# Kernel tuning notes

Measured on AMD Instinct MI355X. Metric: run time of the kernel, lower is better.

The kernel has to match this reference:

```python
import jax, jax.numpy as jnp
import numpy as np

HIDDEN = 2048
INTER = 8192
RANK = 16
SPARSITY_RATIO = 0.5
MAINTAIN_CHANNELS = 10


def setup_inputs() -> dict:
    key = jax.random.key(0)
    ks = jax.random.split(key, 7)
    B, S = 4, 2048
    x1 = jax.random.normal(ks[0], (B, S, HIDDEN), dtype=jnp.float32)
    # Linear weights stored transposed (in_features, out_features), bias=False
    w_up = jax.random.normal(ks[1], (HIDDEN, INTER), dtype=jnp.float32) / np.sqrt(HIDDEN)
    w_up_lora_a = jax.random.normal(ks[2], (HIDDEN, RANK), dtype=jnp.float32) / np.sqrt(HIDDEN)
    w_up_lora_b = jax.random.normal(ks[3], (RANK, INTER), dtype=jnp.float32) / np.sqrt(RANK)
    w_down = jax.random.normal(ks[4], (INTER, HIDDEN), dtype=jnp.float32) / np.sqrt(INTER)
    w_down_lora_a = jax.random.normal(ks[5], (INTER, RANK), dtype=jnp.float32) / np.sqrt(INTER)
    w_down_lora_b = jax.random.normal(ks[6], (RANK, HIDDEN), dtype=jnp.float32) / np.sqrt(RANK)
    return {
        "x1": x1,
        "w_up": w_up,
        "w_up_lora_a": w_up_lora_a,
        "w_up_lora_b": w_up_lora_b,
        "w_down": w_down,
        "w_down_lora_a": w_down_lora_a,
        "w_down_lora_b": w_down_lora_b,
    }


def reference(x1, w_up, w_up_lora_a, w_up_lora_b, w_down, w_down_lora_a, w_down_lora_b):
    # up projection: dense + low-rank LoRA
    y1 = x1 @ w_up + (x1 @ w_up_lora_a) @ w_up_lora_b          # [B, S, I]
    x2 = jax.nn.relu(y1)                                        # activation_forward='relu'
    # down projection: dense + low-rank LoRA
    y2 = x2 @ w_down + (x2 @ w_down_lora_a) @ w_down_lora_b    # [B, S, H]
    # sparse-save path: per-channel zero counts, keep k channels with FEWEST zeros
    zero_counts = jnp.sum(x2 == 0, axis=-2)                     # [B, I]
    k = min(int(SPARSITY_RATIO * x2.shape[-1]), MAINTAIN_CHANNELS)
    _, topk_indices = jax.lax.top_k(-zero_counts, k)            # smallest counts -> [B, k]
    # per-batch gather of selected channels (replaces Python loop in original)
    x2_save = jnp.take_along_axis(x2, topk_indices[:, None, :], axis=-1)  # [B, S, k]
    return y2, x2_save
```

## Files before the change

### kernel.cpp

```cpp
#include <hip/hip_runtime.h>
#include <stdint.h>

#define HIDDEN 2048
#define INTER 8192
#define RANK 16
#define BATCH 4
#define SEQ 2048
#define MROWS (BATCH * SEQ)
#define KSAVE 10
#define FIXCAP (1u << 18)
#define FIX_TAU 1.2e-4f
#define NHALF 4096

typedef unsigned short u16;
typedef __attribute__((ext_vector_type(8))) __bf16 bf16x8;
typedef __attribute__((ext_vector_type(4))) float f32x4;

__device__ __forceinline__ float bf16_to_f32(u16 h) {
    return __uint_as_float(((unsigned int)h) << 16);
}
__device__ __forceinline__ u16 f32_to_bf16(float f) {
    unsigned int u = __float_as_uint(f);
    u += 0x7fffu + ((u >> 16) & 1u);
    return (u16)(u >> 16);
}
__device__ __forceinline__ void split_bf16(float v, u16& h, u16& l) {
    h = f32_to_bf16(v);
    l = f32_to_bf16(v - bf16_to_f32(h));
}

#define TILE_SH (128 * 32)

__device__ __forceinline__ int swz_chunk(int r, int c) {
    return r * 4 + (c ^ ((r >> 1) & 3));
}

template <int NCH>
__device__ __forceinline__ void stage_tileN(const u16* g, int ldk, u16* lds, int tid) {
    int wid = tid >> 6, lane = tid & 63;
#pragma unroll
    for (int c0 = 0; c0 < NCH; c0 += 512) {
        int ch = c0 + wid * 64 + lane;
        int r = ch >> 2;
        int c = (ch & 3) ^ ((r >> 1) & 3);
        const u16* src = g + (size_t)r * ldk + c * 8;
        u16* dst = lds + (size_t)(c0 + wid * 64) * 8;
        __builtin_amdgcn_global_load_lds(
            (const __attribute__((address_space(1))) void*)src,
            (__attribute__((address_space(3))) void*)dst, 16, 0, 0);
    }
}

__device__ __forceinline__ bf16x8 read_frag(const u16* lds, int r, int q) {
    return *(const bf16x8*)(lds + swz_chunk(r, q) * 8);
}

__global__ __launch_bounds__(512) void gemm_up_mfma3(
    const float* __restrict__ x1,
    const u16* __restrict__ wth, const u16* __restrict__ wtl,
    const float* __restrict__ t1, const float* __restrict__ upB,
    u16* __restrict__ x2, int* __restrict__ counts,
    unsigned* __restrict__ fixctr, unsigned* __restrict__ fixlist,
    int noff)
{
    __shared__ u16 Ah[TILE_SH], Al[TILE_SH];
    __shared__ u16 Bh[2 * TILE_SH], Bl[2 * TILE_SH];
    int tid = threadIdx.x, lane = tid & 63, wid = tid >> 6;
    int wr = wid >> 2, wc = wid & 3;
    int col = lane & 15, q = lane >> 4;

    int bid = blockIdx.y * gridDim.x + blockIdx.x;
    int g = bid >> 8, within = bid & 255;
    int nb = g * 4 + (within & 3);
    int mb = within >> 2;
    int m0 = mb * 128, n0l = nb * 256, n0g = noff + n0l;

    f32x4 acc[4][4];
#pragma unroll
    for (int i = 0; i < 4; ++i)
#pragma unroll
        for (int j = 0; j < 4; ++j) acc[i][j] = (f32x4){0.f, 0.f, 0.f, 0.f};

    const float* ga = x1 + (size_t)m0 * HIDDEN;
    const u16* gb_h = wth + (size_t)n0l * HIDDEN;
    const u16* gb_l = wtl + (size_t)n0l * HIDDEN;
    int f4 = tid & 7;
    int rA = tid >> 3;

    for (int k0 = 0; k0 < HIDDEN; k0 += 32) {
        stage_tileN<1024>(gb_h + k0, HIDDEN, Bh, tid);
        stage_tileN<1024>(gb_l + k0, HIDDEN, Bl, tid);
#pragma unroll
        for (int h = 0; h < 2; ++h) {
            int row = rA + h * 64;
            float4 v = *(const float4*)(ga + (size_t)row * HIDDEN + k0 + f4 * 4);
            unsigned hx0 = __float_as_uint(v.x) & 0xffff0000u;
            unsigned hx1 = __float_as_uint(v.y) & 0xffff0000u;
            unsigned hx2 = __float_as_uint(v.z) & 0xffff0000u;
            unsigned hx3 = __float_as_uint(v.w) & 0xffff0000u;
            float l0 = v.x - __uint_as_float(hx0);
            float l1 = v.y - __uint_as_float(hx1);
            float l2 = v.z - __uint_as_float(hx2);
            float l3 = v.w - __uint_as_float(hx3);
            unsigned lo0 = __float_as_uint(l0) & 0xffff0000u;
            unsigned lo1 = __float_as_uint(l1) & 0xffff0000u;
            unsigned lo2 = __float_as_uint(l2) & 0xffff0000u;
            unsigned lo3 = __float_as_uint(l3) & 0xffff0000u;
            uint2 hp = {(hx0 >> 16) | hx1, (hx2 >> 16) | hx3};
            uint2 lp = {(lo0 >> 16) | lo1, (lo2 >> 16) | lo3};
            int pos = swz_chunk(row, f4 >> 1) * 8 + (f4 & 1) * 4;
            *(uint2*)(Ah + pos) = hp;
            *(uint2*)(Al + pos) = lp;
        }
        __syncthreads();
        bf16x8 ah[4], al[4];
#pragma unroll
        for (int i = 0; i < 4; ++i) {
            int r = wr * 64 + i * 16 + col;
            ah[i] = read_frag(Ah, r, q);
            al[i] = read_frag(Al, r, q);
        }
#pragma unroll
        for (int j = 0; j < 4; ++j) {
            int rr = wc * 64 + j * 16 + col;
            bf16x8 bh = read_frag(Bh, rr, q);
            bf16x8 bl = read_frag(Bl, rr, q);
#pragma unroll
            for (int i = 0; i < 4; ++i) {
                acc[i][j] = __builtin_amdgcn_mfma_f32_16x16x32_bf16(ah[i], bh, acc[i][j], 0, 0, 0);
                acc[i][j] = __builtin_amdgcn_mfma_f32_16x16x32_bf16(al[i], bh, acc[i][j], 0, 0, 0);
                acc[i][j] = __builtin_amdgcn_mfma_f32_16x16x32_bf16(ah[i], bl, acc[i][j], 0, 0, 0);
            }
        }
        __syncthreads();
    }

    for (int idx = tid; idx < 4096; idx += 512) {
        int r = idx >> 5, c16 = idx & 31;
        float tv = (c16 < RANK) ? t1[(size_t)(m0 + r) * RANK + c16] : 0.f;
        u16 th, tl2;
        split_bf16(tv, th, tl2);
        int pos = swz_chunk(r, c16 >> 3) * 8 + (c16 & 7);
        Ah[pos] = th; Al[pos] = tl2;
    }
    for (int idx = tid; idx < 8192; idx += 512) {
        int r = idx >> 5, c16 = idx & 31;
        float uv = (c16 < RANK) ? upB[(size_t)c16 * INTER + n0g + r] : 0.f;
        u16 uh, ul;
        split_bf16(uv, uh, ul);
        int pos = swz_chunk(r, c16 >> 3) * 8 + (c16 & 7);
        Bh[pos] = uh; Bl[pos] = ul;
    }
    __syncthreads();
    {
        bf16x8 ah[4], al[4];
#pragma unroll
        for (int i = 0; i < 4; ++i) {
            int r = wr * 64 + i * 16 + col;
            ah[i] = read_frag(Ah, r, q);
            al[i] = read_frag(Al, r, q);
        }
#pragma unroll
        for (int j = 0; j < 4; ++j) {
            int rr = wc * 64 + j * 16 + col;
            bf16x8 bh = read_frag(Bh, rr, q);
            bf16x8 bl = read_frag(Bl, rr, q);
#pragma unroll
            for (int i = 0; i < 4; ++i) {
                acc[i][j] = __builtin_amdgcn_mfma_f32_16x16x32_bf16(ah[i], bh, acc[i][j], 0, 0, 0);
                acc[i][j] = __builtin_amdgcn_mfma_f32_16x16x32_bf16(al[i], bh, acc[i][j], 0, 0, 0);
                acc[i][j] = __builtin_amdgcn_mfma_f32_16x16x32_bf16(ah[i], bl, acc[i][j], 0, 0, 0);
            }
        }
    }

    int b = m0 >> 11;
#pragma unroll
    for (int j = 0; j < 4; ++j) {
        int n = n0g + wc * 64 + j * 16 + col;
        int zc = 0;
#pragma unroll
        for (int i = 0; i < 4; ++i) {
#pragma unroll
            for (int reg = 0; reg < 4; ++reg) {
                int m = m0 + wr * 64 + i * 16 + q * 4 + reg;
                float v = acc[i][j][reg];
                if (fabsf(v) < FIX_TAU) {
                    unsigned slot = atomicAdd(fixctr, 1u);
                    if (slot < FIXCAP) fixlist[slot] = ((unsigned)m << 13) | (unsigned)n;
                }
                zc += (v <= 0.f) ? 1 : 0;
                float rv = v > 0.f ? v : 0.f;
                x2[(size_t)m * INTER + n] = f32_to_bf16(rv);
            }
        }
        zc += __shfl_down(zc, 32);
        zc += __shfl_down(zc, 16);
        if (lane < 16) atomicAdd(&counts[b * INTER + n], zc);
    }
}

__global__ __launch_bounds__(512) void gemm_down_mfma2(
    const u16* __restrict__ x2, const u16* __restrict__ wdt,
    const float* __restrict__ t2, const float* __restrict__ dnB,
    float* __restrict__ out)
{
    __shared__ u16 As[TILE_SH];
    __shared__ u16 Bs[2 * TILE_SH];
    int tid = threadIdx.x, lane = tid & 63, wid = tid >> 6;
    int wr = wid >> 2, wc = wid & 3;
    int col = lane & 15, q = lane >> 4;
    int m0 = blockIdx.y * 128, n0 = blockIdx.x * 256;

    f32x4 acc[4][4];
#pragma unroll
    for (int i = 0; i < 4; ++i)
#pragma unroll
        for (int j = 0; j < 4; ++j) acc[i][j] = (f32x4){0.f, 0.f, 0.f, 0.f};

    const u16* ga = x2 + (size_t)m0 * INTER;
    const u16* gb = wdt + (size_t)n0 * INTER;

    for (int k0 = 0; k0 < INTER; k0 += 32) {
        stage_tileN<512>(ga + k0, INTER, As, tid);
        stage_tileN<1024>(gb + k0, INTER, Bs, tid);
        __syncthreads();
        bf16x8 af[4];
#pragma unroll
        for (int i = 0; i < 4; ++i) af[i] = read_frag(As, wr * 64 + i * 16 + col, q);
#pragma unroll
        for (int j = 0; j < 4; ++j) {
            bf16x8 bf = read_frag(Bs, wc * 64 + j * 16 + col, q);
#pragma unroll
            for (int i = 0; i < 4; ++i)
                acc[i][j] = __builtin_amdgcn_mfma_f32_16x16x32_bf16(af[i], bf, acc[i][j], 0, 0, 0);
        }
        __syncthreads();
    }

    for (int idx = tid; idx < 4096; idx += 512) {
        int r = idx >> 5, c16 = idx & 31;
        float tv = (c16 < RANK) ? t2[(size_t)(m0 + r) * RANK + c16] : 0.f;
        int pos = swz_chunk(r, c16 >> 3) * 8 + (c16 & 7);
        As[pos] = f32_to_bf16(tv);
    }
    for (int idx = tid; idx < 8192; idx += 512) {
        int r = idx >> 5, c16 = idx & 31;
        float uv = (c16 < RANK) ? dnB[(size_t)c16 * HIDDEN + n0 + r] : 0.f;
        int pos = swz_chunk(r, c16 >> 3) * 8 + (c16 & 7);
        Bs[pos] = f32_to_bf16(uv);
    }
    __syncthreads();
    {
        bf16x8 af[4];
#pragma unroll
        for (int i = 0; i < 4; ++i) af[i] = read_frag(As, wr * 64 + i * 16 + col, q);
#pragma unroll
        for (int j = 0; j < 4; ++j) {
            bf16x8 bf = read_frag(Bs, wc * 64 + j * 16 + col, q);
#pragma unroll
            for (int i = 0; i < 4; ++i)
                acc[i][j] = __builtin_amdgcn_mfma_f32_16x16x32_bf16(af[i], bf, acc[i][j], 0, 0, 0);
        }
    }
#pragma unroll
    for (int i = 0; i < 4; ++i)
#pragma unroll
        for (int j = 0; j < 4; ++j) {
            int n = n0 + wc * 64 + j * 16 + col;
#pragma unroll
            for (int reg = 0; reg < 4; ++reg) {
                int m = m0 + wr * 64 + i * 16 + q * 4 + reg;
                out[(size_t)m * HIDDEN + n] = acc[i][j][reg];
            }
        }
}

__global__ __launch_bounds__(256) void fixup_kernel(
    const float* __restrict__ x1, const float* __restrict__ w_up,
    const float* __restrict__ t1, const float* __restrict__ upB,
    const unsigned* __restrict__ fixctr, const unsigned* __restrict__ fixlist,
    u16* __restrict__ x2, int* __restrict__ counts)
{
    unsigned n_items = *fixctr;
    if (n_items > FIXCAP) n_items = FIXCAP;
    int lane = threadIdx.x & 63;
    int gwave = blockIdx.x * 4 + (threadIdx.x >> 6);
    int nwaves = gridDim.x * 4;
    for (unsigned it = gwave; it < n_items; it += nwaves) {
        unsigned code = fixlist[it];
        int m = code >> 13, n = code & 8191;
        float s = 0.f;
        const float* xr = x1 + (size_t)m * HIDDEN;
        for (int k = lane; k < HIDDEN; k += 64)
            s = fmaf(xr[k], w_up[(size_t)k * INTER + n], s);
#pragma unroll
        for (int off = 32; off > 0; off >>= 1) s += __shfl_down(s, off);
        if (lane == 0) {
            float lo = 0.f;
#pragma unroll
            for (int r = 0; r < RANK; ++r)
                lo = fmaf(t1[(size_t)m * RANK + r], upB[(size_t)r * INTER + n], lo);
            float y = s + lo;
            int oldz = (x2[(size_t)m * INTER + n] == 0) ? 1 : 0;
            int newz = (y <= 0.f) ? 1 : 0;
            if (newz != oldz) atomicAdd(&counts[(m >> 11) * INTER + n], newz - oldz);
            x2[(size_t)m * INTER + n] = f32_to_bf16(y > 0.f ? y : 0.f);
        }
    }
}

template <bool SPLIT>
__global__ __launch_bounds__(256) void transpose_cvt(
    const float* __restrict__ in, u16* __restrict__ outh, u16* __restrict__ outl,
    int R, int C)
{
    __shared__ float t[32][33];
    int x = threadIdx.x & 31, y = threadIdx.x >> 5;
    int r0 = blockIdx.y * 32, c0 = blockIdx.x * 32;
#pragma unroll
    for (int p = 0; p < 4; ++p)
        t[y + p * 8][x] = in[(size_t)(r0 + y + p * 8) * C + c0 + x];
    __syncthreads();
#pragma unroll
    for (int p = 0; p < 4; ++p) {
        float v = t[x][y + p * 8];
        u16 h = f32_to_bf16(v);
        outh[(size_t)(c0 + y + p * 8) * R + r0 + x] = h;
        if (SPLIT)
            outl[(size_t)(c0 + y + p * 8) * R + r0 + x] = f32_to_bf16(v - bf16_to_f32(h));
    }
}

__global__ __launch_bounds__(256) void rowdot16_f32(
    const float* __restrict__ X, const float* __restrict__ A,
    float* __restrict__ T, int K)
{
    __shared__ float red[256][RANK + 1];
    int m = blockIdx.x;
    const float* xr = X + (size_t)m * K;
    float acc[RANK];
#pragma unroll
    for (int r = 0; r < RANK; ++r) acc[r] = 0.f;
    for (int k = threadIdx.x; k < K; k += 256) {
        float xv = xr[k];
        const float* ar = A + (size_t)k * RANK;
#pragma unroll
        for (int r = 0; r < RANK; ++r) acc[r] = fmaf(xv, ar[r], acc[r]);
    }
#pragma unroll
    for (int r = 0; r < RANK; ++r) red[threadIdx.x][r] = acc[r];
    __syncthreads();
    for (int off = 128; off > 0; off >>= 1) {
        if (threadIdx.x < off) {
#pragma unroll
            for (int r = 0; r < RANK; ++r)
                red[threadIdx.x][r] += red[threadIdx.x + off][r];
        }
        __syncthreads();
    }
    if (threadIdx.x < RANK) T[(size_t)m * RANK + threadIdx.x] = red[0][threadIdx.x];
}

__global__ __launch_bounds__(256) void rowdot16_bf16(
    const u16* __restrict__ X, const float* __restrict__ A,
    float* __restrict__ T, int K)
{
    __shared__ float red[256][RANK + 1];
    int m = blockIdx.x;
    const u16* xr = X + (size_t)m * K;
    float acc[RANK];
#pragma unroll
    for (int r = 0; r < RANK; ++r) acc[r] = 0.f;
    for (int k = threadIdx.x * 8; k < K; k += 256 * 8) {
        uint4 p = *(const uint4*)(xr + k);
        unsigned w_[4] = {p.x, p.y, p.z, p.w};
#pragma unroll
        for (int e = 0; e < 4; ++e) {
            float v0 = bf16_to_f32((u16)(w_[e] & 0xffffu));
            float v1 = bf16_to_f32((u16)(w_[e] >> 16));
            const float* ar0 = A + (size_t)(k + 2 * e) * RANK;
            const float* ar1 = A + (size_t)(k + 2 * e + 1) * RANK;
#pragma unroll
            for (int r = 0; r < RANK; ++r)
                acc[r] = fmaf(v0, ar0[r], fmaf(v1, ar1[r], acc[r]));
        }
    }
#pragma unroll
    for (int r = 0; r < RANK; ++r) red[threadIdx.x][r] = acc[r];
    __syncthreads();
    for (int off = 128; off > 0; off >>= 1) {
        if (threadIdx.x < off) {
#pragma unroll
            for (int r = 0; r < RANK; ++r)
                red[threadIdx.x][r] += red[threadIdx.x + off][r];
        }
        __syncthreads();
    }
    if (threadIdx.x < RANK) T[(size_t)m * RANK + threadIdx.x] = red[0][threadIdx.x];
}

#define BM 128
#define BN 128
#define BK 16
#define TM 8

__global__ __launch_bounds__(256) void gemm_up_f32(
    const float* __restrict__ A, const float* __restrict__ B,
    const float* __restrict__ Tl, const float* __restrict__ Bl,
    u16* __restrict__ C, int M, int N, int K)
{
    __shared__ float As[BK][BM + 4];
    __shared__ float Bs[BK][BN];
    int tid = threadIdx.x;
    int tx = tid % 16, ty = tid / 16;
    int m0 = blockIdx.y * BM, n0 = blockIdx.x * BN;
    const float* Ab = A + (size_t)m0 * K;
    const float* Bb = B + n0;
    float acc[TM][8];
#pragma unroll
    for (int i = 0; i < TM; ++i)
#pragma unroll
        for (int j = 0; j < 8; ++j) acc[i][j] = 0.f;

    int arow = tid >> 2, acol = (tid & 3) * 4;
    int brow = tid >> 5, bcol = (tid & 31) * 4;

    for (int k0 = 0; k0 < K; k0 += BK) {
#pragma unroll
        for (int h = 0; h < 2; ++h) {
            int r = arow + h * 64;
            float4 v = *(const float4*)(Ab + (size_t)r * K + k0 + acol);
            As[acol + 0][r] = v.x; As[acol + 1][r] = v.y;
            As[acol + 2][r] = v.z; As[acol + 3][r] = v.w;
        }
#pragma unroll
        for (int h = 0; h < 2; ++h) {
            int r = brow + h * 8;
            float4 v = *(const float4*)(Bb + (size_t)(k0 + r) * N + bcol);
            *(float4*)&Bs[r][bcol] = v;
        }
        __syncthreads();
#pragma unroll
        for (int kk = 0; kk < BK; ++kk) {
            float a[TM], b[8];
#pragma unroll
            for (int i = 0; i < TM; i += 4) *(float4*)&a[i] = *(const float4*)&As[kk][ty * TM + i];
            *(float4*)&b[0] = *(const float4*)&Bs[kk][tx * 4];
            *(float4*)&b[4] = *(const float4*)&Bs[kk][64 + tx * 4];
#pragma unroll
            for (int i = 0; i < TM; ++i)
#pragma unroll
                for (int j = 0; j < 8; ++j)
                    acc[i][j] = fmaf(a[i], b[j], acc[i][j]);
        }
        __syncthreads();
    }
#pragma unroll
    for (int r = 0; r < RANK; ++r) {
        float bv[8];
#pragma unroll
        for (int j = 0; j < 4; ++j) {
            bv[j]     = Bl[(size_t)r * N + n0 + tx * 4 + j];
            bv[4 + j] = Bl[(size_t)r * N + n0 + 64 + tx * 4 + j];
        }
#pragma unroll
        for (int i = 0; i < TM; ++i) {
            float tv = Tl[(size_t)(m0 + ty * TM + i) * RANK + r];
#pragma unroll
            for (int j = 0; j < 8; ++j) acc[i][j] = fmaf(tv, bv[j], acc[i][j]);
        }
    }
#pragma unroll
    for (int i = 0; i < TM; ++i) {
        int m = m0 + ty * TM + i;
        float v[8];
#pragma unroll
        for (int j = 0; j < 8; ++j) { float x = acc[i][j]; v[j] = x > 0.f ? x : 0.f; }
        uint2 p0, p1;
        p0.x = (unsigned)f32_to_bf16(v[0]) | ((unsigned)f32_to_bf16(v[1]) << 16);
        p0.y = (unsigned)f32_to_bf16(v[2]) | ((unsigned)f32_to_bf16(v[3]) << 16);
        p1.x = (unsigned)f32_to_bf16(v[4]) | ((unsigned)f32_to_bf16(v[5]) << 16);
        p1.y = (unsigned)f32_to_bf16(v[6]) | ((unsigned)f32_to_bf16(v[7]) << 16);
        *(uint2*)(C + (size_t)m * N + n0 + tx * 4) = p0;
        *(uint2*)(C + (size_t)m * N + n0 + 64 + tx * 4) = p1;
    }
}

__global__ __launch_bounds__(256) void gemm_down_f32(
    const u16* __restrict__ A, const float* __restrict__ B,
    const float* __restrict__ Tl, const float* __restrict__ Bl,
    float* __restrict__ C, int M, int N, int K)
{
    __shared__ float As[BK][BM + 4];
    __shared__ float Bs[BK][BN];
    int tid = threadIdx.x;
    int tx = tid % 16, ty = tid / 16;
    int m0 = blockIdx.y * BM, n0 = blockIdx.x * BN;
    const u16* Ab = A + (size_t)m0 * K;
    const float* Bb = B + n0;
    float acc[TM][8];
#pragma unroll
    for (int i = 0; i < TM; ++i)
#pragma unroll
        for (int j = 0; j < 8; ++j) acc[i][j] = 0.f;

    int arow = tid >> 1, ahalf = (tid & 1) * 8;
    int brow = tid >> 5, bcol = (tid & 31) * 4;

    for (int k0 = 0; k0 < K; k0 += BK) {
        {
            uint4 v = *(const uint4*)(Ab + (size_t)arow * K + k0 + ahalf);
            unsigned int w_[4] = {v.x, v.y, v.z, v.w};
#pragma unroll
            for (int qq = 0; qq < 4; ++qq) {
                As[ahalf + 2 * qq + 0][arow] = bf16_to_f32((u16)(w_[qq] & 0xffffu));
                As[ahalf + 2 * qq + 1][arow] = bf16_to_f32((u16)(w_[qq] >> 16));
            }
        }
#pragma unroll
        for (int h = 0; h < 2; ++h) {
            int r = brow + h * 8;
            float4 v = *(const float4*)(Bb + (size_t)(k0 + r) * N + bcol);
            *(float4*)&Bs[r][bcol] = v;
        }
        __syncthreads();
#pragma unroll
        for (int kk = 0; kk < BK; ++kk) {
            float a[TM], b[8];
#pragma unroll
            for (int i = 0; i < TM; i += 4) *(float4*)&a[i] = *(const float4*)&As[kk][ty * TM + i];
            *(float4*)&b[0] = *(const float4*)&Bs[kk][tx * 4];
            *(float4*)&b[4] = *(const float4*)&Bs[kk][64 + tx * 4];
#pragma unroll
            for (int i = 0; i < TM; ++i)
#pragma unroll
                for (int j = 0; j < 8; ++j)
                    acc[i][j] = fmaf(a[i], b[j], acc[i][j]);
        }
        __syncthreads();
    }
#pragma unroll
    for (int r = 0; r < RANK; ++r) {
        float bv[8];
#pragma unroll
        for (int j = 0; j < 4; ++j) {
            bv[j]     = Bl[(size_t)r * N + n0 + tx * 4 + j];
            bv[4 + j] = Bl[(size_t)r * N + n0 + 64 + tx * 4 + j];
        }
#pragma unroll
        for (int i = 0; i < TM; ++i) {
            float tv = Tl[(size_t)(m0 + ty * TM + i) * RANK + r];
#pragma unroll
            for (int j = 0; j < 8; ++j) acc[i][j] = fmaf(tv, bv[j], acc[i][j]);
        }
    }
#pragma unroll
    for (int i = 0; i < TM; ++i) {
        int m = m0 + ty * TM + i;
        *(float4*)(C + (size_t)m * N + n0 + tx * 4)      = *(float4*)&acc[i][0];
        *(float4*)(C + (size_t)m * N + n0 + 64 + tx * 4) = *(float4*)&acc[i][4];
    }
}

__global__ __launch_bounds__(256) void gemm_down_mfma(
    const u16* __restrict__ x2, const u16* __restrict__ wdt,
    const float* __restrict__ t2, const float* __restrict__ dnB,
    float* __restrict__ out)
{
    __shared__ u16 As[TILE_SH], Bs[TILE_SH];
    int tid = threadIdx.x, lane = tid & 63, wid = tid >> 6;
    int wr = wid >> 1, wc = wid & 1;
    int col = lane & 15, q = lane >> 4;
    int m0 = blockIdx.y * 128, n0 = blockIdx.x * 128;

    f32x4 acc[4][4];
#pragma unroll
    for (int i = 0; i < 4; ++i)
#pragma unroll
        for (int j = 0; j < 4; ++j) acc[i][j] = (f32x4){0.f, 0.f, 0.f, 0.f};

    const u16* ga = x2 + (size_t)m0 * INTER;
    const u16* gb = wdt + (size_t)n0 * INTER;

    for (int k0 = 0; k0 < INTER; k0 += 32) {
        {
            int wid4 = tid >> 6, lane4 = tid & 63;
#pragma unroll
            for (int h = 0; h < 2; ++h) {
                int ch = h * 256 + wid4 * 64 + lane4;
                int r = ch >> 2;
                int c = (ch & 3) ^ ((r >> 1) & 3);
                const u16* srcA = ga + k0 + (size_t)r * INTER + c * 8;
                u16* dstA = As + (size_t)(h * 256 + wid4 * 64) * 8;
                __builtin_amdgcn_global_load_lds(
                    (const __attribute__((address_space(1))) void*)srcA,
                    (__attribute__((address_space(3))) void*)dstA, 16, 0, 0);
                const u16* srcB = gb + k0 + (size_t)r * INTER + c * 8;
                u16* dstB = Bs + (size_t)(h * 256 + wid4 * 64) * 8;
                __builtin_amdgcn_global_load_lds(
                    (const __attribute__((address_space(1))) void*)srcB,
                    (__attribute__((address_space(3))) void*)dstB, 16, 0, 0);
            }
        }
        __syncthreads();
        bf16x8 af[4];
#pragma unroll
        for (int i = 0; i < 4; ++i) af[i] = read_frag(As, wr * 64 + i * 16 + col, q);
#pragma unroll
        for (int j = 0; j < 4; ++j) {
            bf16x8 bf = read_frag(Bs, wc * 64 + j * 16 + col, q);
#pragma unroll
            for (int i = 0; i < 4; ++i)
                acc[i][j] = __builtin_amdgcn_mfma_f32_16x16x32_bf16(af[i], bf, acc[i][j], 0, 0, 0);
        }
        __syncthreads();
    }
    for (int idx = tid; idx < 128 * 32; idx += 256) {
        int r = idx >> 5, c16 = idx & 31;
        float tv = (c16 < RANK) ? t2[(size_t)(m0 + r) * RANK + c16] : 0.f;
        float uv = (c16 < RANK) ? dnB[(size_t)c16 * HIDDEN + n0 + r] : 0.f;
        int pos = swz_chunk(r, c16 >> 3) * 8 + (c16 & 7);
        As[pos] = f32_to_bf16(tv);
        Bs[pos] = f32_to_bf16(uv);
    }
    __syncthreads();
    {
        bf16x8 af[4];
#pragma unroll
        for (int i = 0; i < 4; ++i) af[i] = read_frag(As, wr * 64 + i * 16 + col, q);
#pragma unroll
        for (int j = 0; j < 4; ++j) {
            bf16x8 bf = read_frag(Bs, wc * 64 + j * 16 + col, q);
#pragma unroll
            for (int i = 0; i < 4; ++i)
                acc[i][j] = __builtin_amdgcn_mfma_f32_16x16x32_bf16(af[i], bf, acc[i][j], 0, 0, 0);
        }
    }
#pragma unroll
    for (int i = 0; i < 4; ++i)
#pragma unroll
        for (int j = 0; j < 4; ++j) {
            int n = n0 + wc * 64 + j * 16 + col;
#pragma unroll
            for (int reg = 0; reg < 4; ++reg) {
                int m = m0 + wr * 64 + i * 16 + q * 4 + reg;
                out[(size_t)m * HIDDEN + n] = acc[i][j][reg];
            }
        }
}

__global__ __launch_bounds__(256) void count_zeros(
    const u16* __restrict__ X2, int* __restrict__ counts)
{
    int i = blockIdx.x * 256 + threadIdx.x;
    int b = blockIdx.y;
    int s0 = blockIdx.z * 256;
    const u16* p = X2 + ((size_t)(b * SEQ + s0)) * INTER + i;
    int c = 0;
    for (int s = 0; s < 256; ++s) c += (p[(size_t)s * INTER] == 0) ? 1 : 0;
    atomicAdd(&counts[b * INTER + i], c);
}

__global__ __launch_bounds__(256) void topk10(
    const int* __restrict__ counts, int* __restrict__ topidx)
{
    __shared__ int keys[INTER];
    __shared__ int red[256];
    int b = blockIdx.x;
    for (int i = threadIdx.x; i < INTER; i += 256)
        keys[i] = (counts[b * INTER + i] << 13) | i;
    __syncthreads();
    for (int sel = 0; sel < KSAVE; ++sel) {
        int best = 0x7fffffff;
        for (int i = threadIdx.x; i < INTER; i += 256)
            best = min(best, keys[i]);
        red[threadIdx.x] = best;
        __syncthreads();
        for (int off = 128; off > 0; off >>= 1) {
            if (threadIdx.x < off) red[threadIdx.x] = min(red[threadIdx.x], red[threadIdx.x + off]);
            __syncthreads();
        }
        int bestkey = red[0];
        if (threadIdx.x == 0) {
            topidx[b * KSAVE + sel] = bestkey & 0x1fff;
            keys[bestkey & 0x1fff] = 0x7fffffff;
        }
        __syncthreads();
    }
}

__global__ __launch_bounds__(256) void gather_save(
    const u16* __restrict__ X2, const int* __restrict__ topidx,
    float* __restrict__ out2)
{
    int t = blockIdx.x * 256 + threadIdx.x;
    if (t >= BATCH * SEQ * KSAVE) return;
    int j = t % KSAVE;
    int s = (t / KSAVE) % SEQ;
    int b = t / (KSAVE * SEQ);
    int idx = topidx[b * KSAVE + j];
    out2[t] = bf16_to_f32(X2[((size_t)(b * SEQ + s)) * INTER + idx]);
}

extern "C" void kernel_launch(void* const* d_in, const int* in_sizes, int n_in,
                              void* d_out, int out_size, void* d_ws, size_t ws_size,
                              hipStream_t stream)
{
    const float* x1   = (const float*)d_in[0];
    const float* w_up = (const float*)d_in[1];
    const float* upA  = (const float*)d_in[2];
    const float* upB  = (const float*)d_in[3];
    const float* w_dn = (const float*)d_in[4];
    const float* dnA  = (const float*)d_in[5];
    const float* dnB  = (const float*)d_in[6];
    float* out = (float*)d_out;
    char* ws = (char*)d_ws;

    const size_t X2B   = (size_t)MROWS * INTER * 2;
    const size_t WHALF = (size_t)NHALF * HIDDEN * 2;
    const size_t WSPL  = (size_t)HIDDEN * INTER * 2;
    const size_t TB    = (size_t)MROWS * RANK * 4;
    const size_t CNTB  = (size_t)BATCH * INTER * 4;

    size_t fast_need = X2B + 2 * WHALF + 2 * TB + CNTB + 512 + 4 * (size_t)FIXCAP;
    size_t mid_need  = X2B + WSPL + 2 * TB + CNTB + 512;

    u16* x2 = (u16*)ws;
    size_t off = X2B;

    if (ws_size >= fast_need) {
        u16* wth = (u16*)(ws + off);            off += WHALF;
        u16* wtl = (u16*)(ws + off);            off += WHALF;
        float* t1 = (float*)(ws + off);         off += TB;
        float* t2 = (float*)(ws + off);         off += TB;
        int* counts = (int*)(ws + off);         off += CNTB;
        int* topidx = (int*)(ws + off);         off += 256;
        unsigned* fixctr = (unsigned*)(ws + off); off += 256;
        unsigned* fixlist = (unsigned*)(ws + off);
        u16* wdt = wth;

        hipMemsetAsync(counts, 0, CNTB, stream);
        hipMemsetAsync(fixctr, 0, 4, stream);

        rowdot16_f32<<<MROWS, 256, 0, stream>>>(x1, upA, t1, HIDDEN);

        for (int half = 0; half < 2; ++half) {
            int noff = half * NHALF;
            transpose_cvt<true><<<dim3(NHALF / 32, HIDDEN / 32), 256, 0, stream>>>(
                w_up + noff, wth, wtl, HIDDEN, INTER);
            gemm_up_mfma3<<<dim3(NHALF / 256, MROWS / 128), 512, 0, stream>>>(
                x1, wth, wtl, t1, upB, x2, counts, fixctr, fixlist, noff);
        }
        fixup_kernel<<<256, 256, 0, stream>>>(x1, w_up, t1, upB, fixctr, fixlist, x2, counts);

        topk10<<<BATCH, 256, 0, stream>>>(counts, topidx);
        gather_save<<<(BATCH * SEQ * KSAVE + 255) / 256, 256, 0, stream>>>(
            x2, topidx, out + (size_t)MROWS * HIDDEN);

        transpose_cvt<false><<<dim3(HIDDEN / 32, INTER / 32), 256, 0, stream>>>(
            w_dn, wdt, nullptr, INTER, HIDDEN);
        rowdot16_bf16<<<MROWS, 256, 0, stream>>>(x2, dnA, t2, INTER);
        gemm_down_mfma2<<<dim3(HIDDEN / 256, MROWS / 128), 512, 0, stream>>>(
            x2, wdt, t2, dnB, out);
    } else if (ws_size >= mid_need) {
        u16* wdt = (u16*)(ws + off);            off += WSPL;
        float* t1 = (float*)(ws + off);         off += TB;
        float* t2 = (float*)(ws + off);         off += TB;
        int* counts = (int*)(ws + off);         off += CNTB;
        int* topidx = (int*)(ws + off);

        hipMemsetAsync(counts, 0, CNTB, stream);
        rowdot16_f32<<<MROWS, 256, 0, stream>>>(x1, upA, t1, HIDDEN);
        gemm_up_f32<<<dim3(INTER / BN, MROWS / BM), 256, 0, stream>>>(
            x1, w_up, t1, upB, x2, MROWS, INTER, HIDDEN);
        count_zeros<<<dim3(INTER / 256, BATCH, SEQ / 256), 256, 0, stream>>>(x2, counts);
        topk10<<<BATCH, 256, 0, stream>>>(counts, topidx);
        gather_save<<<(BATCH * SEQ * KSAVE + 255) / 256, 256, 0, stream>>>(
            x2, topidx, out + (size_t)MROWS * HIDDEN);
        transpose_cvt<false><<<dim3(HIDDEN / 32, INTER / 32), 256, 0, stream>>>(
            w_dn, wdt, nullptr, INTER, HIDDEN);
        rowdot16_bf16<<<MROWS, 256, 0, stream>>>(x2, dnA, t2, INTER);
        gemm_down_mfma<<<dim3(HIDDEN / 128, MROWS / 128), 256, 0, stream>>>(
            x2, wdt, t2, dnB, out);
    } else {
        float* t1 = (float*)(ws + off);         off += TB;
        float* t2 = (float*)(ws + off);         off += TB;
        int* counts = (int*)(ws + off);         off += CNTB;
        int* topidx = (int*)(ws + off);

        hipMemsetAsync(counts, 0, CNTB, stream);
        rowdot16_f32<<<MROWS, 256, 0, stream>>>(x1, upA, t1, HIDDEN);
        gemm_up_f32<<<dim3(INTER / BN, MROWS / BM), 256, 0, stream>>>(
            x1, w_up, t1, upB, x2, MROWS, INTER, HIDDEN);
        count_zeros<<<dim3(INTER / 256, BATCH, SEQ / 256), 256, 0, stream>>>(x2, counts);
        topk10<<<BATCH, 256, 0, stream>>>(counts, topidx);
        gather_save<<<(BATCH * SEQ * KSAVE + 255) / 256, 256, 0, stream>>>(
            x2, topidx, out + (size_t)MROWS * HIDDEN);
        rowdot16_bf16<<<MROWS, 256, 0, stream>>>(x2, dnA, t2, INTER);
        gemm_down_f32<<<dim3(HIDDEN / BN, MROWS / BM), 256, 0, stream>>>(
            x2, w_dn, t2, dnB, out, MROWS, HIDDEN, INTER);
    }
}
```

Before: 2.258 ms.

## Shrink up-GEMM tile to 128x128 and replace LoRA rowdots with thread-per-row kernels

The up-projection GEMM moves from 512 threads with 128x256 tiles to 256 threads with 128x128 tiles. This halves LDS use per block and doubles the block count, and the A-tile global loads are now batched before conversion. The LoRA rank-16 projections switch from block-per-row reductions to thread-per-row kernels: split-K with a combine pass for t1, and split-K with atomics for t2. The mid-path rowdot kernel is simplified to scalar loads. The change also shrinks the fixup capacity, which risks overflow if many elements need fixing, and the atomics make t2 accumulation order nondeterministic.

```diff
diff --git a/kernel.cpp b/kernel.cpp
--- a/kernel.cpp
+++ b/kernel.cpp
@@ -8,7 +8,7 @@
 #define SEQ 2048
 #define MROWS (BATCH * SEQ)
 #define KSAVE 10
-#define FIXCAP (1u << 18)
+#define FIXCAP (1u << 16)
 #define FIX_TAU 1.2e-4f
 #define NHALF 4096
 
@@ -33,6 +33,20 @@
 
 __device__ __forceinline__ int swz_chunk(int r, int c) {
     return r * 4 + (c ^ ((r >> 1) & 3));
+}
+
+__device__ __forceinline__ void stage_tile256(const u16* g, int ldk, u16* lds, int wid, int lane) {
+#pragma unroll
+    for (int h = 0; h < 2; ++h) {
+        int ch = h * 256 + wid * 64 + lane;
+        int r = ch >> 2;
+        int c = (ch & 3) ^ ((r >> 1) & 3);
+        const u16* src = g + (size_t)r * ldk + c * 8;
+        u16* dst = lds + (size_t)(h * 256 + wid * 64) * 8;
+        __builtin_amdgcn_global_load_lds(
+            (const __attribute__((address_space(1))) void*)src,
+            (__attribute__((address_space(3))) void*)dst, 16, 0, 0);
+    }
 }
 
 template <int NCH>
@@ -55,7 +69,7 @@
     return *(const bf16x8*)(lds + swz_chunk(r, q) * 8);
 }
 
-__global__ __launch_bounds__(512) void gemm_up_mfma3(
+__global__ __launch_bounds__(256) void gemm_up_mfma2(
     const float* __restrict__ x1,
     const u16* __restrict__ wth, const u16* __restrict__ wtl,
     const float* __restrict__ t1, const float* __restrict__ upB,
@@ -63,17 +77,16 @@
     unsigned* __restrict__ fixctr, unsigned* __restrict__ fixlist,
     int noff)
 {
-    __shared__ u16 Ah[TILE_SH], Al[TILE_SH];
-    __shared__ u16 Bh[2 * TILE_SH], Bl[2 * TILE_SH];
+    __shared__ u16 Ah[TILE_SH], Al[TILE_SH], Bh[TILE_SH], Bl[TILE_SH];
     int tid = threadIdx.x, lane = tid & 63, wid = tid >> 6;
-    int wr = wid >> 2, wc = wid & 3;
+    int wr = wid >> 1, wc = wid & 1;
     int col = lane & 15, q = lane >> 4;
 
     int bid = blockIdx.y * gridDim.x + blockIdx.x;
-    int g = bid >> 8, within = bid & 255;
-    int nb = g * 4 + (within & 3);
-    int mb = within >> 2;
-    int m0 = mb * 128, n0l = nb * 256, n0g = noff + n0l;
+    int g = bid >> 9, within = bid & 511;
+    int nb = g * 8 + (within & 7);
+    int mb = within >> 3;
+    int m0 = mb * 128, n0l = nb * 128, n0g = noff + n0l;
 
     f32x4 acc[4][4];
 #pragma unroll
@@ -88,20 +101,23 @@
     int rA = tid >> 3;
 
     for (int k0 = 0; k0 < HIDDEN; k0 += 32) {
-        stage_tileN<1024>(gb_h + k0, HIDDEN, Bh, tid);
-        stage_tileN<1024>(gb_l + k0, HIDDEN, Bl, tid);
-#pragma unroll
-        for (int h = 0; h < 2; ++h) {
-            int row = rA + h * 64;
-            float4 v = *(const float4*)(ga + (size_t)row * HIDDEN + k0 + f4 * 4);
-            unsigned hx0 = __float_as_uint(v.x) & 0xffff0000u;
-            unsigned hx1 = __float_as_uint(v.y) & 0xffff0000u;
-            unsigned hx2 = __float_as_uint(v.z) & 0xffff0000u;
-            unsigned hx3 = __float_as_uint(v.w) & 0xffff0000u;
-            float l0 = v.x - __uint_as_float(hx0);
-            float l1 = v.y - __uint_as_float(hx1);
-            float l2 = v.z - __uint_as_float(hx2);
-            float l3 = v.w - __uint_as_float(hx3);
+        stage_tile256(gb_h + k0, HIDDEN, Bh, wid, lane);
+        stage_tile256(gb_l + k0, HIDDEN, Bl, wid, lane);
+        float4 v[4];
+#pragma unroll
+        for (int h = 0; h < 4; ++h)
+            v[h] = *(const float4*)(ga + (size_t)(rA + h * 32) * HIDDEN + k0 + f4 * 4);
+#pragma unroll
+        for (int h = 0; h < 4; ++h) {
+            int row = rA + h * 32;
+            unsigned hx0 = __float_as_uint(v[h].x) & 0xffff0000u;
+            unsigned hx1 = __float_as_uint(v[h].y) & 0xffff0000u;
+            unsigned hx2 = __float_as_uint(v[h].z) & 0xffff0000u;
+            unsigned hx3 = __float_as_uint(v[h].w) & 0xffff0000u;
+            float l0 = v[h].x - __uint_as_float(hx0);
+            float l1 = v[h].y - __uint_as_float(hx1);
+            float l2 = v[h].z - __uint_as_float(hx2);
+            float l3 = v[h].w - __uint_as_float(hx3);
             unsigned lo0 = __float_as_uint(l0) & 0xffff0000u;
             unsigned lo1 = __float_as_uint(l1) & 0xffff0000u;
             unsigned lo2 = __float_as_uint(l2) & 0xffff0000u;
@@ -135,21 +151,15 @@
         __syncthreads();
     }
 
-    for (int idx = tid; idx < 4096; idx += 512) {
+    for (int idx = tid; idx < 4096; idx += 256) {
         int r = idx >> 5, c16 = idx & 31;
         float tv = (c16 < RANK) ? t1[(size_t)(m0 + r) * RANK + c16] : 0.f;
-        u16 th, tl2;
+        float uv = (c16 < RANK) ? upB[(size_t)c16 * INTER + n0g + r] : 0.f;
+        u16 th, tl2, uh, ul;
         split_bf16(tv, th, tl2);
-        int pos = swz_chunk(r, c16 >> 3) * 8 + (c16 & 7);
-        Ah[pos] = th; Al[pos] = tl2;
-    }
-    for (int idx = tid; idx < 8192; idx += 512) {
-        int r = idx >> 5, c16 = idx & 31;
-        float uv = (c16 < RANK) ? upB[(size_t)c16 * INTER + n0g + r] : 0.f;
-        u16 uh, ul;
         split_bf16(uv, uh, ul);
         int pos = swz_chunk(r, c16 >> 3) * 8 + (c16 & 7);
-        Bh[pos] = uh; Bl[pos] = ul;
+        Ah[pos] = th; Al[pos] = tl2; Bh[pos] = uh; Bl[pos] = ul;
     }
     __syncthreads();
     {
@@ -310,6 +320,70 @@
     }
 }
 
+__global__ __launch_bounds__(256) void lora_t1_part(
+    const float* __restrict__ X, const float* __restrict__ A,
+    float* __restrict__ Tpart)
+{
+    int m = blockIdx.x * 256 + threadIdx.x;
+    int k0 = blockIdx.y * (HIDDEN / 2);
+    const float* xr = X + (size_t)m * HIDDEN + k0;
+    const float* Ab = A + (size_t)k0 * RANK;
+    float acc[RANK];
+#pragma unroll
+    for (int r = 0; r < RANK; ++r) acc[r] = 0.f;
+    for (int k = 0; k < HIDDEN / 2; k += 4) {
+        float4 xv = *(const float4*)(xr + k);
+        const float* ar = Ab + (size_t)k * RANK;
+        float xs[4] = {xv.x, xv.y, xv.z, xv.w};
+#pragma unroll
+        for (int e = 0; e < 4; ++e)
+#pragma unroll
+            for (int r = 0; r < RANK; ++r)
+                acc[r] = fmaf(xs[e], ar[e * RANK + r], acc[r]);
+    }
+    float* dst = Tpart + ((size_t)blockIdx.y * MROWS + m) * RANK;
+#pragma unroll
+    for (int r = 0; r < RANK; ++r) dst[r] = acc[r];
+}
+
+__global__ __launch_bounds__(256) void lora_t1_combine(
+    const float* __restrict__ Tpart, float* __restrict__ T)
+{
+    int i = blockIdx.x * 256 + threadIdx.x;
+    T[i] = Tpart[i] + Tpart[(size_t)MROWS * RANK + i];
+}
+
+__global__ __launch_bounds__(256) void lora_t2_atomic(
+    const u16* __restrict__ X, const float* __restrict__ A,
+    float* __restrict__ T)
+{
+    int m = blockIdx.x * 256 + threadIdx.x;
+    const int kn = INTER / 8;
+    int k0 = blockIdx.y * kn;
+    const u16* xr = X + (size_t)m * INTER + k0;
+    const float* Ab = A + (size_t)k0 * RANK;
+    float acc[RANK];
+#pragma unroll
+    for (int r = 0; r < RANK; ++r) acc[r] = 0.f;
+    for (int k = 0; k < kn; k += 8) {
+        uint4 p = *(const uint4*)(xr + k);
+        unsigned w_[4] = {p.x, p.y, p.z, p.w};
+        const float* ar = Ab + (size_t)k * RANK;
+#pragma unroll
+        for (int e = 0; e < 4; ++e) {
+            float v0 = bf16_to_f32((u16)(w_[e] & 0xffffu));
+            float v1 = bf16_to_f32((u16)(w_[e] >> 16));
+#pragma unroll
+            for (int r = 0; r < RANK; ++r)
+                acc[r] = fmaf(v0, ar[(2 * e) * RANK + r],
+                         fmaf(v1, ar[(2 * e + 1) * RANK + r], acc[r]));
+        }
+    }
+#pragma unroll
+    for (int r = 0; r < RANK; ++r)
+        atomicAdd(&T[(size_t)m * RANK + r], acc[r]);
+}
+
 template <bool SPLIT>
 __global__ __launch_bounds__(256) void transpose_cvt(
     const float* __restrict__ in, u16* __restrict__ outh, u16* __restrict__ outl,
@@ -372,19 +446,11 @@
     float acc[RANK];
 #pragma unroll
     for (int r = 0; r < RANK; ++r) acc[r] = 0.f;
-    for (int k = threadIdx.x * 8; k < K; k += 256 * 8) {
-        uint4 p = *(const uint4*)(xr + k);
-        unsigned w_[4] = {p.x, p.y, p.z, p.w};
-#pragma unroll
-        for (int e = 0; e < 4; ++e) {
-            float v0 = bf16_to_f32((u16)(w_[e] & 0xffffu));
-            float v1 = bf16_to_f32((u16)(w_[e] >> 16));
-            const float* ar0 = A + (size_t)(k + 2 * e) * RANK;
-            const float* ar1 = A + (size_t)(k + 2 * e + 1) * RANK;
-#pragma unroll
-            for (int r = 0; r < RANK; ++r)
-                acc[r] = fmaf(v0, ar0[r], fmaf(v1, ar1[r], acc[r]));
-        }
+    for (int k = threadIdx.x; k < K; k += 256) {
+        float xv = bf16_to_f32(xr[k]);
+        const float* ar = A + (size_t)k * RANK;
+#pragma unroll
+        for (int r = 0; r < RANK; ++r) acc[r] = fmaf(xv, ar[r], acc[r]);
     }
 #pragma unroll
     for (int r = 0; r < RANK; ++r) red[threadIdx.x][r] = acc[r];
@@ -584,25 +650,8 @@
     const u16* gb = wdt + (size_t)n0 * INTER;
 
     for (int k0 = 0; k0 < INTER; k0 += 32) {
-        {
-            int wid4 = tid >> 6, lane4 = tid & 63;
-#pragma unroll
-            for (int h = 0; h < 2; ++h) {
-                int ch = h * 256 + wid4 * 64 + lane4;
-                int r = ch >> 2;
-                int c = (ch & 3) ^ ((r >> 1) & 3);
-                const u16* srcA = ga + k0 + (size_t)r * INTER + c * 8;
-                u16* dstA = As + (size_t)(h * 256 + wid4 * 64) * 8;
-                __builtin_amdgcn_global_load_lds(
-                    (const __attribute__((address_space(1))) void*)srcA,
-                    (__attribute__((address_space(3))) void*)dstA, 16, 0, 0);
-                const u16* srcB = gb + k0 + (size_t)r * INTER + c * 8;
-                u16* dstB = Bs + (size_t)(h * 256 + wid4 * 64) * 8;
-                __builtin_amdgcn_global_load_lds(
-                    (const __attribute__((address_space(1))) void*)srcB,
-                    (__attribute__((address_space(3))) void*)dstB, 16, 0, 0);
-            }
-        }
+        stage_tile256(ga + k0, INTER, As, wid, lane);
+        stage_tile256(gb + k0, INTER, Bs, wid, lane);
         __syncthreads();
         bf16x8 af[4];
 #pragma unroll
@@ -723,7 +772,8 @@
     const size_t TB    = (size_t)MROWS * RANK * 4;
     const size_t CNTB  = (size_t)BATCH * INTER * 4;
 
-    size_t fast_need = X2B + 2 * WHALF + 2 * TB + CNTB + 512 + 4 * (size_t)FIXCAP;
+    size_t fast_need = X2B + 2 * WHALF + 2 * TB + 2 * TB  + CNTB + 512
+                     + 4 * (size_t)FIXCAP;
     size_t mid_need  = X2B + WSPL + 2 * TB + CNTB + 512;
 
     u16* x2 = (u16*)ws;
@@ -734,6 +784,7 @@
         u16* wtl = (u16*)(ws + off);            off += WHALF;
         float* t1 = (float*)(ws + off);         off += TB;
         float* t2 = (float*)(ws + off);         off += TB;
+        float* t1part = (float*)(ws + off);     off += 2 * TB;
         int* counts = (int*)(ws + off);         off += CNTB;
         int* topidx = (int*)(ws + off);         off += 256;
         unsigned* fixctr = (unsigned*)(ws + off); off += 256;
@@ -742,17 +793,21 @@
 
         hipMemsetAsync(counts, 0, CNTB, stream);
         hipMemsetAsync(fixctr, 0, 4, stream);
-
-        rowdot16_f32<<<MROWS, 256, 0, stream>>>(x1, upA, t1, HIDDEN);
+        hipMemsetAsync(t2, 0, TB, stream);
+
+        lora_t1_part<<<dim3(MROWS / 256, 2), 256, 0, stream>>>(x1, upA, t1part);
+        lora_t1_combine<<<MROWS * RANK / 256, 256, 0, stream>>>(t1part, t1);
 
         for (int half = 0; half < 2; ++half) {
             int noff = half * NHALF;
             transpose_cvt<true><<<dim3(NHALF / 32, HIDDEN / 32), 256, 0, stream>>>(
                 w_up + noff, wth, wtl, HIDDEN, INTER);
-            gemm_up_mfma3<<<dim3(NHALF / 256, MROWS / 128), 512, 0, stream>>>(
+            gemm_up_mfma2<<<dim3(NHALF / 128, MROWS / 128), 256, 0, stream>>>(
                 x1, wth, wtl, t1, upB, x2, counts, fixctr, fixlist, noff);
         }
         fixup_kernel<<<256, 256, 0, stream>>>(x1, w_up, t1, upB, fixctr, fixlist, x2, counts);
+
+        lora_t2_atomic<<<dim3(MROWS / 256, 8), 256, 0, stream>>>(x2, dnA, t2);
 
         topk10<<<BATCH, 256, 0, stream>>>(counts, topidx);
         gather_save<<<(BATCH * SEQ * KSAVE + 255) / 256, 256, 0, stream>>>(
@@ -760,7 +815,6 @@
 
         transpose_cvt<false><<<dim3(HIDDEN / 32, INTER / 32), 256, 0, stream>>>(
             w_dn, wdt, nullptr, INTER, HIDDEN);
-        rowdot16_bf16<<<MROWS, 256, 0, stream>>>(x2, dnA, t2, INTER);
         gemm_down_mfma2<<<dim3(HIDDEN / 256, MROWS / 128), 512, 0, stream>>>(
             x2, wdt, t2, dnB, out);
     } else if (ws_size >= mid_need) {
```

Result: faster. 1.826 ms (-19.1%).
